# Kernel optimization log

Hardware: AMD Instinct MI355X
Metric: run time of the kernel (lower is better)

Reference implementation:

```python
import jax, jax.numpy as jnp
import numpy as np

R = 4            # search_range -> (2R+1)^2 = 81 displacement channels
B, C, H, W = 8, 128, 128, 224
CH_IN = C + (2 * R + 1) ** 2  # 209


def _conv2d(x, w, b):
    # x: [B,Cin,H,W], w: [Cout,Cin,3,3] -> SAME padding, stride 1
    y = jax.lax.conv_general_dilated(
        x, w, window_strides=(1, 1), padding='SAME',
        dimension_numbers=('NCHW', 'OIHW', 'NCHW'))
    return y + b[None, :, None, None]


def _leaky(x):
    return jnp.where(x >= 0, x, 0.1 * x)


def _correlation(x1, x2):
    # FlowNet-style correlation, kernel_size=1, stride1=stride2=1,
    # pad=max_displacement=R; normalized by number of elements (= C).
    b, c, h, w = x1.shape
    x2p = jnp.pad(x2, ((0, 0), (0, 0), (R, R), (R, R)))
    outs = []
    for dy in range(2 * R + 1):          # fixed 9x9 displacement window
        for dx in range(2 * R + 1):
            shifted = x2p[:, :, dy:dy + h, dx:dx + w]
            outs.append(jnp.mean(x1 * shifted, axis=1))  # [B,H,W]
    return jnp.stack(outs, axis=1)       # [B,81,H,W]


def _xavier_uniform(key, shape):
    fan_out = shape[0] * shape[2] * shape[3]
    fan_in = shape[1] * shape[2] * shape[3]
    a = jnp.sqrt(6.0 / (fan_in + fan_out))
    return jax.random.uniform(key, shape, jnp.float32, -a, a)


def setup_inputs() -> dict:
    key = jax.random.key(0)
    ks = jax.random.split(key, 10)
    return {
        'x1': jax.random.normal(ks[0], (B, C, H, W), jnp.float32),
        'x2': jax.random.normal(ks[1], (B, C, H, W), jnp.float32),
        'w1': _xavier_uniform(ks[2], (64, CH_IN, 3, 3)),
        'b1': jnp.zeros((64,), jnp.float32),
        'w2': _xavier_uniform(ks[3], (64, 64, 3, 3)),
        'b2': jnp.zeros((64,), jnp.float32),
        'w3': _xavier_uniform(ks[4], (32, 64, 3, 3)),
        'b3': jnp.zeros((32,), jnp.float32),
        'w4': _xavier_uniform(ks[5], (2, 32, 3, 3)),
        'b4': jnp.zeros((2,), jnp.float32),
    }


def reference(x1, x2, w1, b1, w2, b2, w3, b3, w4, b4):
    corr = _correlation(x1, x2)                 # [B,81,H,W]
    h = jnp.concatenate([x1, corr], axis=1)     # [B,209,H,W]
    h = _leaky(_conv2d(h, w1, b1))
    h = _leaky(_conv2d(h, w2, b2))
    h = _leaky(_conv2d(h, w3, b3))
    flow = _conv2d(h, w4, b4)                   # [B,2,H,W]
    return flow
```

## Files before the change

kernel.cpp:

```cpp
#include <hip/hip_runtime.h>
#include <hip/hip_bf16.h>
#include <cstddef>

#define BN 8
#define CCH 128
#define HH 128
#define WW 224
#define ND 81
#define CINP1 224

typedef __attribute__((ext_vector_type(8))) short short8_t;
typedef __attribute__((ext_vector_type(4))) float float4_t;

static __device__ __forceinline__ unsigned short f2bf(float f) {
  __hip_bfloat16 h = __float2bfloat16(f);
  return *(unsigned short*)&h;
}
static __device__ __forceinline__ float bf2f(short s) {
  unsigned u = ((unsigned)(unsigned short)s) << 16;
  return __uint_as_float(u);
}

__global__ __launch_bounds__(256) void convert_x1(
    const float* __restrict__ x1, uint4* __restrict__ a0q) {
  const int g = blockIdx.x * 256 + threadIdx.x;
  const int hw = HH * WW;
  const int b = g / hw, px = g - b * hw;
  const float* src = x1 + (size_t)b * CCH * hw + px;

  uint4 zero; zero.x = zero.y = zero.z = zero.w = 0u;
#pragma unroll
  for (int cq = 0; cq < 16; ++cq) {
    unsigned r[4];
#pragma unroll
    for (int j = 0; j < 4; ++j) {
      const int c = cq * 8 + j * 2;
      const float f0 = src[(size_t)(c + 0) * hw];
      const float f1 = src[(size_t)(c + 1) * hw];
      r[j] = (unsigned)f2bf(f0) | ((unsigned)f2bf(f1) << 16);
    }
    uint4 u; u.x = r[0]; u.y = r[1]; u.z = r[2]; u.w = r[3];
    a0q[(size_t)g * 28 + cq] = u;
  }
  a0q[(size_t)g * 28 + 26] = zero;
  a0q[(size_t)g * 28 + 27] = zero;
}

__global__ __launch_bounds__(512, 2) void corr_mfma(
    const float* __restrict__ x2,
    const uint4* __restrict__ a0q,
    __hip_bfloat16* __restrict__ a0) {
  __shared__ uint4 sB[4 * 576];
  const int tid = threadIdx.x;
  const int lane = tid & 63, w = tid >> 6;
  const int m = lane & 15, q = lane >> 4;
  const int x0 = blockIdx.x * 16, y0 = blockIdx.y * 16, b = blockIdx.z;
  const int hw = HH * WW;

  float4_t acc[2][9][2];
#pragma unroll
  for (int yy = 0; yy < 2; ++yy)
#pragma unroll
    for (int d = 0; d < 9; ++d)
#pragma unroll
      for (int t = 0; t < 2; ++t) acc[yy][d][t] = (float4_t)0.0f;

  for (int cb = 0; cb < 4; ++cb) {
    __syncthreads();
    for (int s = tid; s < 2304; s += 512) {
      const int qs = s / 576, rc = s - qs * 576;
      const int r = rc / 24, c = rc - r * 24;
      const int gy = y0 - 4 + r, gx = x0 - 4 + c;
      uint4 u; u.x = u.y = u.z = u.w = 0u;
      if (gy >= 0 && gy < HH && gx >= 0 && gx < WW) {
        const float* p2 =
            x2 + (size_t)(b * CCH + cb * 32 + qs * 8) * hw + gy * WW + gx;
        unsigned rr[4];
#pragma unroll
        for (int j = 0; j < 4; ++j) {
          const float f0 = p2[(size_t)(2 * j + 0) * hw];
          const float f1 = p2[(size_t)(2 * j + 1) * hw];
          rr[j] = (unsigned)f2bf(f0) | ((unsigned)f2bf(f1) << 16);
        }
        u.x = rr[0]; u.y = rr[1]; u.z = rr[2]; u.w = rr[3];
      }
      sB[s] = u;
    }
    __syncthreads();

    uint4 afr[2];
#pragma unroll
    for (int yy = 0; yy < 2; ++yy) {
      const int y = y0 + 2 * w + yy;
      afr[yy] = a0q[((size_t)(b * HH + y) * WW + x0 + m) * 28 + cb * 4 + q];
    }

#pragma unroll
    for (int yy = 0; yy < 2; ++yy) {
      const short8_t af = *(const short8_t*)&afr[yy];
#pragma unroll
      for (int dyi = 0; dyi < 9; ++dyi) {
        const int r = 2 * w + yy + dyi;
#pragma unroll
        for (int t = 0; t < 2; ++t) {
          const short8_t bf =
              *(const short8_t*)&sB[q * 576 + r * 24 + 8 * t + m];
          acc[yy][dyi][t] = __builtin_amdgcn_mfma_f32_16x16x32_bf16(
              af, bf, acc[yy][dyi][t], 0, 0, 0);
        }
      }
    }
  }

  const float sc = 1.0f / 128.0f;
#pragma unroll
  for (int yy = 0; yy < 2; ++yy) {
    const int y = y0 + 2 * w + yy;
    __hip_bfloat16* dst = a0 + ((size_t)(b * HH + y) * WW + x0) * CINP1;
#pragma unroll
    for (int dyi = 0; dyi < 9; ++dyi) {
#pragma unroll
      for (int t = 0; t < 2; ++t) {
#pragma unroll
        for (int r = 0; r < 4; ++r) {
          const int mm = 4 * q + r;
          const int nabs = 8 * t + m;
          const int dxi = nabs - mm;
          if (dxi >= 0 && dxi <= 8 && (t == 0 || m >= 8)) {
            dst[(size_t)mm * CINP1 + 128 + dyi * 9 + dxi] =
                __float2bfloat16(acc[yy][dyi][t][r] * sc);
          }
        }
      }
    }
  }
}

__global__ void repack_w_bf16(const float* __restrict__ w,
                              __hip_bfloat16* __restrict__ wt,
                              int COUT, int CIN, int CINPAD) {
  const int idx = blockIdx.x * 256 + threadIdx.x;
  const int n = 9 * COUT * CINPAD;
  if (idx >= n) return;
  const int t = idx / (COUT * CINPAD);
  const int rem = idx - t * (COUT * CINPAD);
  const int co = rem / CINPAD;
  const int ci = rem - co * CINPAD;
  const float v = (ci < CIN) ? w[(size_t)(co * CIN + ci) * 9 + t] : 0.0f;
  wt[idx] = __float2bfloat16(v);
}

template <int CINPAD, int COUT, bool LEAKY>
__global__ __launch_bounds__(256, 2) void conv_mfma(
    const uint4* __restrict__ inq,
    const __hip_bfloat16* __restrict__ wt,
    const float* __restrict__ bias,
    __hip_bfloat16* __restrict__ out) {
  constexpr int NT = COUT / 16;
  constexpr int NCB = CINPAD / 32;
  constexpr int QSTRIDE_A = 324;
  __shared__ uint4 sA[4 * QSTRIDE_A];
  __shared__ uint4 sW[4 * 9 * COUT];

  const int tid = threadIdx.x;
  const int lane = tid & 63, w = tid >> 6;
  const int m = lane & 15, q = lane >> 4;
  const int x0 = blockIdx.x * 16, y0 = blockIdx.y * 16, b = blockIdx.z;
  const uint4* wq = (const uint4*)wt;

  float4_t acc[4][NT];
#pragma unroll
  for (int my = 0; my < 4; ++my)
#pragma unroll
    for (int nt = 0; nt < NT; ++nt) acc[my][nt] = (float4_t)0.0f;

  for (int cb = 0; cb < NCB; ++cb) {
    __syncthreads();
    for (int s = tid; s < 324; s += 256) {
      const int pr = s / 18, pc = s - pr * 18;
      const int gy = y0 - 1 + pr, gx = x0 - 1 + pc;
      uint4 c0, c1, c2, c3;
      if (gy >= 0 && gy < HH && gx >= 0 && gx < WW) {
        const size_t base =
            ((size_t)(b * HH + gy) * WW + gx) * (CINPAD / 8) + cb * 4;
        c0 = inq[base + 0]; c1 = inq[base + 1];
        c2 = inq[base + 2]; c3 = inq[base + 3];
      } else {
        c0.x=c0.y=c0.z=c0.w=0u; c1=c0; c2=c0; c3=c0;
      }
      sA[0 * QSTRIDE_A + s] = c0;
      sA[1 * QSTRIDE_A + s] = c1;
      sA[2 * QSTRIDE_A + s] = c2;
      sA[3 * QSTRIDE_A + s] = c3;
    }
    for (int s = tid; s < 9 * COUT; s += 256) {
      const int t = s / COUT, co = s - t * COUT;
      const size_t base = ((size_t)(t * COUT + co) * CINPAD + cb * 32) / 8;
      const uint4 c0 = wq[base + 0], c1 = wq[base + 1];
      const uint4 c2 = wq[base + 2], c3 = wq[base + 3];
      sW[(0 * 9 + t) * COUT + co] = c0;
      sW[(1 * 9 + t) * COUT + co] = c1;
      sW[(2 * 9 + t) * COUT + co] = c2;
      sW[(3 * 9 + t) * COUT + co] = c3;
    }
    __syncthreads();

#pragma unroll
    for (int t = 0; t < 9; ++t) {
      const int dy = t / 3 - 1, dx = t % 3 - 1;
      short8_t bf[NT];
#pragma unroll
      for (int nt = 0; nt < NT; ++nt) {
        bf[nt] = *(const short8_t*)&sW[(q * 9 + t) * COUT + nt * 16 + m];
      }
#pragma unroll
      for (int my = 0; my < 4; ++my) {
        const int row = 4 * w + my + dy + 1;
        const int col = m + dx + 1;
        const short8_t af =
            *(const short8_t*)&sA[q * QSTRIDE_A + row * 18 + col];
#pragma unroll
        for (int nt = 0; nt < NT; ++nt) {
          acc[my][nt] = __builtin_amdgcn_mfma_f32_16x16x32_bf16(
              af, bf[nt], acc[my][nt], 0, 0, 0);
        }
      }
    }
  }

#pragma unroll
  for (int my = 0; my < 4; ++my) {
    const int y = y0 + 4 * w + my;
#pragma unroll
    for (int nt = 0; nt < NT; ++nt) {
      const int co = nt * 16 + m;
      const float bv = bias[co];
#pragma unroll
      for (int r = 0; r < 4; ++r) {
        const int x = x0 + q * 4 + r;
        float v = acc[my][nt][r] + bv;
        if (LEAKY) v = (v >= 0.0f) ? v : 0.1f * v;
        out[((size_t)(b * HH + y) * WW + x) * COUT + co] = __float2bfloat16(v);
      }
    }
  }
}

__global__ __launch_bounds__(256, 2) void conv4_kernel(
    const uint4* __restrict__ inq,
    const __hip_bfloat16* __restrict__ wt,
    const float* __restrict__ bias,
    float* __restrict__ out) {
  __shared__ uint4 sA[4 * 324];
  __shared__ uint4 sW[9 * 2 * 4];
  const int tid = threadIdx.x;
  const int tx = tid & 15, ty = tid >> 4;
  const int x0 = blockIdx.x * 16, y0 = blockIdx.y * 16, b = blockIdx.z;

  for (int s = tid; s < 324; s += 256) {
    const int pr = s / 18, pc = s - pr * 18;
    const int gy = y0 - 1 + pr, gx = x0 - 1 + pc;
    uint4 c0, c1, c2, c3;
    if (gy >= 0 && gy < HH && gx >= 0 && gx < WW) {
      const size_t base = ((size_t)(b * HH + gy) * WW + gx) * 4;
      c0 = inq[base + 0]; c1 = inq[base + 1];
      c2 = inq[base + 2]; c3 = inq[base + 3];
    } else {
      c0.x=c0.y=c0.z=c0.w=0u; c1=c0; c2=c0; c3=c0;
    }
    sA[0 * 324 + s] = c0; sA[1 * 324 + s] = c1;
    sA[2 * 324 + s] = c2; sA[3 * 324 + s] = c3;
  }
  if (tid < 72) sW[tid] = ((const uint4*)wt)[tid];
  __syncthreads();

  float acc0 = bias[0], acc1 = bias[1];
#pragma unroll
  for (int t = 0; t < 9; ++t) {
    const int dy = t / 3 - 1, dx = t % 3 - 1;
    const int row = ty + dy + 1, col = tx + dx + 1;
#pragma unroll
    for (int qi = 0; qi < 4; ++qi) {
      const short8_t a = *(const short8_t*)&sA[qi * 324 + row * 18 + col];
      const short8_t w0 = *(const short8_t*)&sW[(t * 2 + 0) * 4 + qi];
      const short8_t w1 = *(const short8_t*)&sW[(t * 2 + 1) * 4 + qi];
#pragma unroll
      for (int j = 0; j < 8; ++j) {
        const float av = bf2f(a[j]);
        acc0 += av * bf2f(w0[j]);
        acc1 += av * bf2f(w1[j]);
      }
    }
  }
  const int y = y0 + ty, x = x0 + tx;
  out[((size_t)(b * 2 + 0) * HH + y) * WW + x] = acc0;
  out[((size_t)(b * 2 + 1) * HH + y) * WW + x] = acc1;
}

extern "C" void kernel_launch(void* const* d_in, const int* in_sizes, int n_in,
                              void* d_out, int out_size, void* d_ws,
                              size_t ws_size, hipStream_t stream) {
  const float* x1 = (const float*)d_in[0];
  const float* x2 = (const float*)d_in[1];
  const float* w1 = (const float*)d_in[2];
  const float* b1 = (const float*)d_in[3];
  const float* w2 = (const float*)d_in[4];
  const float* b2 = (const float*)d_in[5];
  const float* w3 = (const float*)d_in[6];
  const float* b3 = (const float*)d_in[7];
  const float* w4 = (const float*)d_in[8];
  const float* b4 = (const float*)d_in[9];
  float* out = (float*)d_out;

  char* ws = (char*)d_ws;
  __hip_bfloat16* A0 = (__hip_bfloat16*)ws;
  const size_t A0_BYTES = (size_t)BN * HH * WW * CINP1 * 2;
  __hip_bfloat16* h1 = (__hip_bfloat16*)(ws + A0_BYTES);
  const size_t H1_BYTES = (size_t)BN * HH * WW * 64 * 2;
  __hip_bfloat16* wt1 = (__hip_bfloat16*)(ws + A0_BYTES + H1_BYTES);
  __hip_bfloat16* wt2 = wt1 + 9 * 64 * CINP1;
  __hip_bfloat16* wt3 = wt2 + 9 * 64 * 64;
  __hip_bfloat16* wt4 = wt3 + 9 * 32 * 64;
  __hip_bfloat16* h2 = (__hip_bfloat16*)ws;
  __hip_bfloat16* h3 = (__hip_bfloat16*)(ws + H1_BYTES);

  {
    int n1 = 9 * 64 * CINP1;
    repack_w_bf16<<<(n1 + 255) / 256, 256, 0, stream>>>(w1, wt1, 64, 209, CINP1);
    int n2 = 9 * 64 * 64;
    repack_w_bf16<<<(n2 + 255) / 256, 256, 0, stream>>>(w2, wt2, 64, 64, 64);
    int n3 = 9 * 32 * 64;
    repack_w_bf16<<<(n3 + 255) / 256, 256, 0, stream>>>(w3, wt3, 32, 64, 64);
    int n4 = 9 * 2 * 32;
    repack_w_bf16<<<(n4 + 255) / 256, 256, 0, stream>>>(w4, wt4, 2, 32, 32);
  }

  convert_x1<<<BN * HH * WW / 256, 256, 0, stream>>>(x1, (uint4*)A0);

  corr_mfma<<<dim3(WW / 16, HH / 16, BN), dim3(512), 0, stream>>>(
      x2, (const uint4*)A0, A0);

  const dim3 grid(WW / 16, HH / 16, BN);
  conv_mfma<CINP1, 64, true>
      <<<grid, 256, 0, stream>>>((const uint4*)A0, wt1, b1, h1);
  conv_mfma<64, 64, true>
      <<<grid, 256, 0, stream>>>((const uint4*)h1, wt2, b2, h2);
  conv_mfma<64, 32, true>
      <<<grid, 256, 0, stream>>>((const uint4*)h2, wt3, b3, h3);
  conv4_kernel<<<grid, 256, 0, stream>>>((const uint4*)h3, wt4, b4, out);
}
```

Before: 537.5 us.

## Pre-convert x2 to bf16 channel-packed layout and remap block indices

Adds a kernel that converts x2 once into a bf16 layout packed eight channels per 16-byte word, so the correlation kernel loads whole 16-byte vectors instead of doing strided fp32 loads and converting each halo element repeatedly. This path runs only if the workspace is large enough. The correlation inner loop is also restructured so each shared-memory B fragment is loaded once and reused for both output rows. The conv and correlation grids are flattened with the batch index in the low bits, which changes which tiles run together and may help L2 reuse of weights. In exchange it adds an extra pass over x2 and extra workspace.

Result: no change. 538.8 us (+0.2%).

```diff
diff --git a/kernel.cpp b/kernel.cpp
--- a/kernel.cpp
+++ b/kernel.cpp
@@ -46,15 +46,42 @@
   a0q[(size_t)g * 28 + 27] = zero;
 }
 
+__global__ __launch_bounds__(256) void convert_x2(
+    const float* __restrict__ x2, uint4* __restrict__ x2q) {
+  const int g = blockIdx.x * 256 + threadIdx.x;
+  const int hw = HH * WW;
+  const int b = g / hw, px = g - b * hw;
+  const float* src = x2 + (size_t)b * CCH * hw + px;
+  const size_t plane = (size_t)BN * hw;
+
+#pragma unroll
+  for (int p = 0; p < 16; ++p) {
+    unsigned r[4];
+#pragma unroll
+    for (int j = 0; j < 4; ++j) {
+      const int c = p * 8 + j * 2;
+      const float f0 = src[(size_t)(c + 0) * hw];
+      const float f1 = src[(size_t)(c + 1) * hw];
+      r[j] = (unsigned)f2bf(f0) | ((unsigned)f2bf(f1) << 16);
+    }
+    uint4 u; u.x = r[0]; u.y = r[1]; u.z = r[2]; u.w = r[3];
+    x2q[(size_t)p * plane + g] = u;
+  }
+}
+
 __global__ __launch_bounds__(512, 2) void corr_mfma(
     const float* __restrict__ x2,
+    const uint4* __restrict__ x2q,
     const uint4* __restrict__ a0q,
-    __hip_bfloat16* __restrict__ a0) {
+    __hip_bfloat16* __restrict__ a0,
+    int use_preconv) {
   __shared__ uint4 sB[4 * 576];
   const int tid = threadIdx.x;
   const int lane = tid & 63, w = tid >> 6;
   const int m = lane & 15, q = lane >> 4;
-  const int x0 = blockIdx.x * 16, y0 = blockIdx.y * 16, b = blockIdx.z;
+  const int lin = blockIdx.x;
+  const int b = lin & 7, idx = lin >> 3;
+  const int x0 = (idx % 14) * 16, y0 = (idx / 14) * 16;
   const int hw = HH * WW;
 
   float4_t acc[2][9][2];
@@ -73,16 +100,21 @@
       const int gy = y0 - 4 + r, gx = x0 - 4 + c;
       uint4 u; u.x = u.y = u.z = u.w = 0u;
       if (gy >= 0 && gy < HH && gx >= 0 && gx < WW) {
-        const float* p2 =
-            x2 + (size_t)(b * CCH + cb * 32 + qs * 8) * hw + gy * WW + gx;
-        unsigned rr[4];
-#pragma unroll
-        for (int j = 0; j < 4; ++j) {
-          const float f0 = p2[(size_t)(2 * j + 0) * hw];
-          const float f1 = p2[(size_t)(2 * j + 1) * hw];
-          rr[j] = (unsigned)f2bf(f0) | ((unsigned)f2bf(f1) << 16);
+        if (use_preconv) {
+          u = x2q[(size_t)(cb * 4 + qs) * (BN * hw) +
+                  (size_t)(b * HH + gy) * WW + gx];
+        } else {
+          const float* p2 =
+              x2 + (size_t)(b * CCH + cb * 32 + qs * 8) * hw + gy * WW + gx;
+          unsigned rr[4];
+#pragma unroll
+          for (int j = 0; j < 4; ++j) {
+            const float f0 = p2[(size_t)(2 * j + 0) * hw];
+            const float f1 = p2[(size_t)(2 * j + 1) * hw];
+            rr[j] = (unsigned)f2bf(f0) | ((unsigned)f2bf(f1) << 16);
+          }
+          u.x = rr[0]; u.y = rr[1]; u.z = rr[2]; u.w = rr[3];
         }
-        u.x = rr[0]; u.y = rr[1]; u.z = rr[2]; u.w = rr[3];
       }
       sB[s] = u;
     }
@@ -94,20 +126,25 @@
       const int y = y0 + 2 * w + yy;
       afr[yy] = a0q[((size_t)(b * HH + y) * WW + x0 + m) * 28 + cb * 4 + q];
     }
-
-#pragma unroll
-    for (int yy = 0; yy < 2; ++yy) {
-      const short8_t af = *(const short8_t*)&afr[yy];
-#pragma unroll
-      for (int dyi = 0; dyi < 9; ++dyi) {
-        const int r = 2 * w + yy + dyi;
-#pragma unroll
-        for (int t = 0; t < 2; ++t) {
-          const short8_t bf =
-              *(const short8_t*)&sB[q * 576 + r * 24 + 8 * t + m];
-          acc[yy][dyi][t] = __builtin_amdgcn_mfma_f32_16x16x32_bf16(
-              af, bf, acc[yy][dyi][t], 0, 0, 0);
-        }
+    const short8_t af0 = *(const short8_t*)&afr[0];
+    const short8_t af1 = *(const short8_t*)&afr[1];
+
+#pragma unroll
+    for (int rr = 0; rr < 10; ++rr) {
+      const int r = 2 * w + rr;
+      const short8_t bf0 = *(const short8_t*)&sB[q * 576 + r * 24 + m];
+      const short8_t bf1 = *(const short8_t*)&sB[q * 576 + r * 24 + 8 + m];
+      if (rr <= 8) {
+        acc[0][rr][0] = __builtin_amdgcn_mfma_f32_16x16x32_bf16(
+            af0, bf0, acc[0][rr][0], 0, 0, 0);
+        acc[0][rr][1] = __builtin_amdgcn_mfma_f32_16x16x32_bf16(
+            af0, bf1, acc[0][rr][1], 0, 0, 0);
+      }
+      if (rr >= 1) {
+        acc[1][rr - 1][0] = __builtin_amdgcn_mfma_f32_16x16x32_bf16(
+            af1, bf0, acc[1][rr - 1][0], 0, 0, 0);
+        acc[1][rr - 1][1] = __builtin_amdgcn_mfma_f32_16x16x32_bf16(
+            af1, bf1, acc[1][rr - 1][1], 0, 0, 0);
       }
     }
   }
@@ -165,7 +202,9 @@
   const int tid = threadIdx.x;
   const int lane = tid & 63, w = tid >> 6;
   const int m = lane & 15, q = lane >> 4;
-  const int x0 = blockIdx.x * 16, y0 = blockIdx.y * 16, b = blockIdx.z;
+  const int lin = blockIdx.x;
+  const int b = lin & 7, idx = lin >> 3;
+  const int x0 = (idx % 14) * 16, y0 = (idx / 14) * 16;
   const uint4* wq = (const uint4*)wt;
 
   float4_t acc[4][NT];
@@ -207,7 +246,7 @@
 
 #pragma unroll
     for (int t = 0; t < 9; ++t) {
-      const int dy = t / 3 - 1, dx = t % 3 - 1;
+      const int tr = t / 3, ds = t % 3;
       short8_t bf[NT];
 #pragma unroll
       for (int nt = 0; nt < NT; ++nt) {
@@ -215,10 +254,9 @@
       }
 #pragma unroll
       for (int my = 0; my < 4; ++my) {
-        const int row = 4 * w + my + dy + 1;
-        const int col = m + dx + 1;
+        const int row = 4 * w + my + tr;
         const short8_t af =
-            *(const short8_t*)&sA[q * QSTRIDE_A + row * 18 + col];
+            *(const short8_t*)&sA[q * QSTRIDE_A + row * 18 + m + ds];
 #pragma unroll
         for (int nt = 0; nt < NT; ++nt) {
           acc[my][nt] = __builtin_amdgcn_mfma_f32_16x16x32_bf16(
@@ -321,6 +359,11 @@
   __hip_bfloat16* wt2 = wt1 + 9 * 64 * CINP1;
   __hip_bfloat16* wt3 = wt2 + 9 * 64 * 64;
   __hip_bfloat16* wt4 = wt3 + 9 * 32 * 64;
+  const size_t WT_BYTES = 2 * (9 * 64 * CINP1 + 9 * 64 * 64 + 9 * 32 * 64 +
+                               9 * 2 * 32);
+  const size_t x2n_off = (A0_BYTES + H1_BYTES + WT_BYTES + 255) & ~(size_t)255;
+  const size_t X2N_BYTES = (size_t)BN * HH * WW * CCH * 2;
+  const int preconv = (ws_size >= x2n_off + X2N_BYTES) ? 1 : 0;
   __hip_bfloat16* h2 = (__hip_bfloat16*)ws;
   __hip_bfloat16* h3 = (__hip_bfloat16*)(ws + H1_BYTES);
 
@@ -337,15 +380,20 @@
 
   convert_x1<<<BN * HH * WW / 256, 256, 0, stream>>>(x1, (uint4*)A0);
 
-  corr_mfma<<<dim3(WW / 16, HH / 16, BN), dim3(512), 0, stream>>>(
-      x2, (const uint4*)A0, A0);
-
+  const uint4* x2q = (const uint4*)(ws + x2n_off);
+  if (preconv) {
+    convert_x2<<<BN * HH * WW / 256, 256, 0, stream>>>(x2, (uint4*)x2q);
+  } else {
+    x2q = (const uint4*)A0;
+  }
+  corr_mfma<<<896, 512, 0, stream>>>(x2, x2q, (const uint4*)A0, A0, preconv);
+
+  conv_mfma<CINP1, 64, true>
+      <<<896, 256, 0, stream>>>((const uint4*)A0, wt1, b1, h1);
+  conv_mfma<64, 64, true>
+      <<<896, 256, 0, stream>>>((const uint4*)h1, wt2, b2, h2);
+  conv_mfma<64, 32, true>
+      <<<896, 256, 0, stream>>>((const uint4*)h2, wt3, b3, h3);
   const dim3 grid(WW / 16, HH / 16, BN);
-  conv_mfma<CINP1, 64, true>
-      <<<grid, 256, 0, stream>>>((const uint4*)A0, wt1, b1, h1);
-  conv_mfma<64, 64, true>
-      <<<grid, 256, 0, stream>>>((const uint4*)h1, wt2, b2, h2);
-  conv_mfma<64, 32, true>
-      <<<grid, 256, 0, stream>>>((const uint4*)h2, wt3, b3, h3);
   conv4_kernel<<<grid, 256, 0, stream>>>((const uint4*)h3, wt4, b4, out);
 }
```
